# Kernel optimization log

Measured on AMD Instinct MI355X. Metric: run time of the kernel, lower is better.

Reference implementation:

```python
import jax, jax.numpy as jnp
import numpy as np


def setup_inputs() -> dict:
    key = jax.random.key(0)
    ks = jax.random.split(key, 5)
    B, c_in, c_out, style_d = 8, 128, 128, 512
    D = H = W = 32
    f = 3
    # xavier_uniform-like scale for conv weight
    fan_in = c_in * f * f * f
    fan_out = c_out * f * f * f
    limit = float(np.sqrt(6.0 / (fan_in + fan_out)))
    x = jax.random.normal(ks[0], (B, c_in, D, H, W), dtype=jnp.float32)
    s = jax.random.normal(ks[1], (B, style_d), dtype=jnp.float32)
    w = jax.random.uniform(ks[2], (c_out, c_in, f, f, f), dtype=jnp.float32, minval=-limit, maxval=limit)
    b = jnp.zeros((c_out, 1, 1, 1), dtype=jnp.float32)
    lim_a = float(np.sqrt(1.0 / style_d))
    affine_w = jax.random.uniform(ks[3], (c_in, style_d), dtype=jnp.float32, minval=-lim_a, maxval=lim_a)
    affine_b = jnp.zeros((c_in,), dtype=jnp.float32)
    return {"x": x, "s": s, "w": w, "b": b, "affine_w": affine_w, "affine_b": affine_b}


def _per_sample_conv(xi, wi):
    # xi: [c_in, D, H, W], wi: [c_out, c_in, 3, 3, 3]
    out = jax.lax.conv_general_dilated(
        xi[None],  # [1, c_in, D, H, W]
        wi,
        window_strides=(1, 1, 1),
        padding=((1, 1), (1, 1), (1, 1)),
        dimension_numbers=("NCDHW", "OIDHW", "NCDHW"),
    )
    return out[0]  # [c_out, D, H, W]


def reference(x, s, w, b, affine_w, affine_b):
    # Style -> per-sample channel scales
    style = s @ affine_w.T + affine_b  # [B, c_in]
    # Modulate: [B, c_out, c_in, f, f, f]
    wmod = w[None] * (style[:, None, :, None, None, None] + 1.0)
    # Demodulate
    d = jnp.sqrt(jnp.sum(jnp.square(wmod), axis=(2, 3, 4, 5), keepdims=True) + 1e-8)
    wmod = wmod / d
    # Per-sample conv (equivalent to grouped conv with groups=B)
    out = jax.vmap(_per_sample_conv)(x, wmod)  # [B, c_out, D, H, W]
    return out + b[None]
```

## Files before the change

kernel.cpp:

```cpp
#include <hip/hip_runtime.h>
#include <stdint.h>
#include <stddef.h>

typedef __attribute__((ext_vector_type(8))) short short8;
typedef __attribute__((ext_vector_type(4))) float floatx4;

#define CI 128
#define CO 128
#define SP 32768
#define BATCH 8
#define STYLED 512
#define KV 3456

__device__ __forceinline__ short f2bf(float f) {
    uint32_t u = __builtin_bit_cast(uint32_t, f);
    u = (u + 0x7FFFu + ((u >> 16) & 1u)) >> 16;
    return (short)(u & 0xFFFFu);
}

__global__ void k_style(const float* __restrict__ s, const float* __restrict__ aw,
                        const float* __restrict__ ab, float* __restrict__ m) {
    __shared__ float ssh[STYLED];
    int b = blockIdx.x;
    int i = threadIdx.x;
    for (int r = 0; r < STYLED / 128; ++r) ssh[r * 128 + i] = s[b * STYLED + r * 128 + i];
    __syncthreads();
    float acc = ab[i] + 1.0f;
    const float4* awr = (const float4*)(aw + (size_t)i * STYLED);
    for (int d4 = 0; d4 < STYLED / 4; ++d4) {
        float4 v = awr[d4];
        acc += v.x * ssh[d4 * 4] + v.y * ssh[d4 * 4 + 1] + v.z * ssh[d4 * 4 + 2] + v.w * ssh[d4 * 4 + 3];
    }
    m[b * CI + i] = acc;
}

__global__ void k_wmod(const float* __restrict__ w, const float* __restrict__ m,
                       short* __restrict__ wt) {
    int b = blockIdx.x >> 7;
    int o = blockIdx.x & 127;
    int lane = threadIdx.x;
    const float* wrow = w + (size_t)o * KV;
    const float* mrow = m + b * CI;
    float sum = 0.f;
    for (int e = lane; e < KV; e += 64) {
        int i = e / 27;
        float v = wrow[e] * mrow[i];
        sum += v * v;
    }
    #pragma unroll
    for (int off = 32; off >= 1; off >>= 1) sum += __shfl_xor(sum, off);
    float scale = 1.0f / sqrtf(sum + 1e-8f);
    for (int e = lane; e < KV; e += 64) {
        int i = e / 27;
        int k = e - i * 27;
        float v = wrow[e] * mrow[i] * scale;
        wt[(((size_t)(b * 27 + k) * CO + o) << 7) + i] = f2bf(v);
    }
}

__global__ void k_xt(const float* __restrict__ x, short* __restrict__ xt) {
    __shared__ float t[128][33];
    int bid = blockIdx.x;
    int b = bid >> 10;
    int zy = bid & 1023;
    const float* src = x + (size_t)b * CI * SP + (size_t)zy * 32;
    int tid = threadIdx.x;
    int wlane = tid & 31, irow = tid >> 5;
    for (int it = 0; it < 16; ++it) {
        int i = it * 8 + irow;
        t[i][wlane] = src[(size_t)i * SP + wlane];
    }
    __syncthreads();
    short* dst = xt + ((size_t)(b * SP + zy * 32)) * CI;
    for (int it = 0; it < 2; ++it) {
        int idx = it * 256 + tid;
        int wv = idx >> 4, g = idx & 15;
        short8 v;
        #pragma unroll
        for (int j = 0; j < 8; ++j) v[j] = f2bf(t[g * 8 + j][wv]);
        *(short8*)(dst + (size_t)wv * CI + g * 8) = v;
    }
}

__launch_bounds__(512, 1)
__global__ void k_conv(const short* __restrict__ xt, const short* __restrict__ wt,
                       const float* __restrict__ bias, float* __restrict__ out) {
    __shared__ short lds_x[612 * 40];
    __shared__ short lds_w[2][128 * 40];

    int bid = blockIdx.x;
    int b = bid & 7;
    int t = bid >> 3;
    int z = t & 31;
    int y0 = (t >> 5) * 4;
    int tid = threadIdx.x;
    int lane = tid & 63;
    int wid = tid >> 6;
    int wm = wid & 3;
    int wn = wid >> 2;
    int l15 = lane & 15;
    int lhi = lane >> 4;
    int i8 = lhi * 8;

    floatx4 acc[2][4];
    #pragma unroll
    for (int a = 0; a < 2; ++a)
        #pragma unroll
        for (int c = 0; c < 4; ++c) acc[a][c] = (floatx4){0.f, 0.f, 0.f, 0.f};

    const short* wbase = wt + (size_t)b * 27 * CO * CI;
    int wo = tid >> 2, wq = tid & 3;

    for (int c = 0; c < 4; ++c) {
        __syncthreads();
        for (int it = 0; it < 5; ++it) {
            int idx = it * 512 + tid;
            if (idx < 2448) {
                int h = idx >> 2, q = idx & 3;
                int zh = h / 204; int r = h - zh * 204;
                int yh = r / 34;  int wh = r - yh * 34;
                int zz = z + zh - 1, yy = y0 + yh - 1, ww = wh - 1;
                short8 v = {0, 0, 0, 0, 0, 0, 0, 0};
                if ((unsigned)zz < 32u && (unsigned)yy < 32u && (unsigned)ww < 32u) {
                    v = *(const short8*)(xt + ((size_t)(b * SP + zz * 1024 + yy * 32 + ww)) * CI + c * 32 + q * 8);
                }
                *(short8*)&lds_x[h * 40 + q * 8] = v;
            }
        }
        {
            short8 v = *(const short8*)(wbase + ((size_t)0 * CO + wo) * CI + c * 32 + wq * 8);
            *(short8*)&lds_w[0][wo * 40 + wq * 8] = v;
        }
        __syncthreads();

        for (int tap = 0; tap < 27; ++tap) {
            short8 wreg;
            if (tap < 26) {
                wreg = *(const short8*)(wbase + ((size_t)(tap + 1) * CO + wo) * CI + c * 32 + wq * 8);
            }
            int cur = tap & 1;
            int kd = tap / 9, r9 = tap - kd * 9;
            int kh = r9 / 3, kw = r9 - kh * 3;

            short8 afr[2];
            #pragma unroll
            for (int mf = 0; mf < 2; ++mf)
                afr[mf] = *(const short8*)&lds_w[cur][(wm * 32 + mf * 16 + l15) * 40 + i8];

            #pragma unroll
            for (int nf = 0; nf < 4; ++nf) {
                int n = wn * 64 + nf * 16;
                int yi = n >> 5;
                int wl = (n & 31) + l15;
                int h = (kd * 6 + yi + kh) * 34 + wl + kw;
                short8 bfr = *(const short8*)&lds_x[h * 40 + i8];
                #pragma unroll
                for (int mf = 0; mf < 2; ++mf)
                    acc[mf][nf] = __builtin_amdgcn_mfma_f32_16x16x32_bf16(afr[mf], bfr, acc[mf][nf], 0, 0, 0);
            }

            if (tap < 26) {
                __syncthreads();
                *(short8*)&lds_w[cur ^ 1][wo * 40 + wq * 8] = wreg;
                __syncthreads();
            }
        }
    }

    float bv[2][4];
    #pragma unroll
    for (int mf = 0; mf < 2; ++mf)
        #pragma unroll
        for (int j = 0; j < 4; ++j)
            bv[mf][j] = bias[wm * 32 + mf * 16 + lhi * 4 + j];

    #pragma unroll
    for (int mf = 0; mf < 2; ++mf) {
        int o = wm * 32 + mf * 16 + lhi * 4;
        #pragma unroll
        for (int nf = 0; nf < 4; ++nf) {
            int n = wn * 64 + nf * 16 + l15;
            int yy = y0 + (n >> 5);
            int ww = n & 31;
            size_t obase = ((size_t)(b * CO + o)) * SP + (size_t)z * 1024 + yy * 32 + ww;
            #pragma unroll
            for (int j = 0; j < 4; ++j)
                out[obase + (size_t)j * SP] = acc[mf][nf][j] + bv[mf][j];
        }
    }
}

extern "C" void kernel_launch(void* const* d_in, const int* in_sizes, int n_in,
                              void* d_out, int out_size, void* d_ws, size_t ws_size,
                              hipStream_t stream) {
    const float* x  = (const float*)d_in[0];
    const float* s  = (const float*)d_in[1];
    const float* w  = (const float*)d_in[2];
    const float* bb = (const float*)d_in[3];
    const float* aw = (const float*)d_in[4];
    const float* ab = (const float*)d_in[5];
    float* out = (float*)d_out;

    float* style_m = (float*)d_ws;
    short* wmodT   = (short*)((char*)d_ws + 4096);
    short* xT      = (short*)((char*)d_ws + 4096 + 7077888);

    k_style<<<BATCH, 128, 0, stream>>>(s, aw, ab, style_m);
    k_wmod<<<BATCH * CO, 64, 0, stream>>>(w, style_m, wmodT);
    k_xt<<<BATCH * 1024, 256, 0, stream>>>(x, xT);
    k_conv<<<BATCH * 256, 512, 0, stream>>>(xT, wmodT, bb, out);
}
```

Measured before the change: 359.0 us.

## Use direct global-to-LDS loads with XOR swizzle and larger conv tiles

The conv kernel now fills LDS with global_load_lds DMA-style loads instead of going through registers. Padding reads are redirected to a zeroed page, and XOR-swizzled layouts for both weights and activations replace the padded-stride scheme to avoid bank conflicts. The weight buffer is re-laid out per 32-channel chunk to match. Each block now covers two z-slices, each warp computes 64x64 instead of 32x64, and the two barriers per tap become one. This raises register pressure and leaves half as many blocks, in exchange for more data reuse and fewer VGPR round trips.

Result: faster. 295.9 us (-17.6%).

```diff
diff --git a/kernel.cpp b/kernel.cpp
--- a/kernel.cpp
+++ b/kernel.cpp
@@ -11,6 +11,13 @@
 #define BATCH 8
 #define STYLED 512
 #define KV 3456
+
+typedef __attribute__((address_space(1))) const void gvoid_t;
+typedef __attribute__((address_space(3))) void lvoid_t;
+
+__device__ __forceinline__ void gload16(const void* g, void* l) {
+    __builtin_amdgcn_global_load_lds((gvoid_t*)g, (lvoid_t*)l, 16, 0, 0);
+}
 
 __device__ __forceinline__ short f2bf(float f) {
     uint32_t u = __builtin_bit_cast(uint32_t, f);
@@ -50,11 +57,14 @@
     #pragma unroll
     for (int off = 32; off >= 1; off >>= 1) sum += __shfl_xor(sum, off);
     float scale = 1.0f / sqrtf(sum + 1e-8f);
+    int ophase = (o >> 1) & 3;
     for (int e = lane; e < KV; e += 64) {
         int i = e / 27;
         int k = e - i * 27;
         float v = wrow[e] * mrow[i] * scale;
-        wt[(((size_t)(b * 27 + k) * CO + o) << 7) + i] = f2bf(v);
+        int c = i >> 5, il = i & 31, g = il >> 3, r = il & 7;
+        int gl = g ^ ophase;
+        wt[(((size_t)((b * 4 + c) * 27 + k)) * 128 + o) * 32 + gl * 8 + r] = f2bf(v);
     }
 }
 
@@ -82,107 +92,102 @@
     }
 }
 
-__launch_bounds__(512, 1)
+__launch_bounds__(512, 4)
 __global__ void k_conv(const short* __restrict__ xt, const short* __restrict__ wt,
-                       const float* __restrict__ bias, float* __restrict__ out) {
-    __shared__ short lds_x[612 * 40];
-    __shared__ short lds_w[2][128 * 40];
+                       const float* __restrict__ bias, float* __restrict__ out,
+                       const short* __restrict__ zeropage) {
+    __shared__ short lds_x[816 * 32];
+    __shared__ short lds_w[2][128 * 32];
 
     int bid = blockIdx.x;
     int b = bid & 7;
     int t = bid >> 3;
-    int z = t & 31;
-    int y0 = (t >> 5) * 4;
+    int zt = t & 15, yt = t >> 4;
+    int z0 = zt * 2, y0 = yt * 4;
+
     int tid = threadIdx.x;
     int lane = tid & 63;
     int wid = tid >> 6;
-    int wm = wid & 3;
-    int wn = wid >> 2;
+    int wm = wid >> 2;
+    int wn = wid & 3;
     int l15 = lane & 15;
     int lhi = lane >> 4;
-    int i8 = lhi * 8;
-
-    floatx4 acc[2][4];
-    #pragma unroll
-    for (int a = 0; a < 2; ++a)
+
+    floatx4 acc[4][4];
+    #pragma unroll
+    for (int a = 0; a < 4; ++a)
         #pragma unroll
         for (int c = 0; c < 4; ++c) acc[a][c] = (floatx4){0.f, 0.f, 0.f, 0.f};
 
-    const short* wbase = wt + (size_t)b * 27 * CO * CI;
-    int wo = tid >> 2, wq = tid & 3;
+    const short* wb = wt + (size_t)b * (4 * 27 * 128 * 32);
+    const short* xb = xt + (size_t)b * SP * CI;
 
     for (int c = 0; c < 4; ++c) {
+        for (int j = 0; ; ++j) {
+            int s = wid + 8 * j;
+            if (s >= 51) break;
+            int G = s * 64 + lane;
+            int rowid = G >> 2, g = G & 3;
+            int zh = rowid / 204; int rr = rowid - zh * 204;
+            int yh = rr / 34;     int wh = rr - yh * 34;
+            int zz = z0 + zh - 1, yy = y0 + yh - 1, ww = wh - 1;
+            int q = g ^ ((rowid >> 1) & 3);
+            const short* src;
+            if ((unsigned)zz < 32u && (unsigned)yy < 32u && (unsigned)ww < 32u)
+                src = xb + ((size_t)(zz * 1024 + yy * 32 + ww)) * CI + c * 32 + q * 8;
+            else
+                src = zeropage + q * 8;
+            gload16(src, (void*)((char*)lds_x + s * 1024));
+        }
+        gload16(wb + ((size_t)(c * 27 + 0)) * 4096 + wid * 512 + lane * 8,
+                (void*)((char*)lds_w[0] + wid * 1024));
         __syncthreads();
-        for (int it = 0; it < 5; ++it) {
-            int idx = it * 512 + tid;
-            if (idx < 2448) {
-                int h = idx >> 2, q = idx & 3;
-                int zh = h / 204; int r = h - zh * 204;
-                int yh = r / 34;  int wh = r - yh * 34;
-                int zz = z + zh - 1, yy = y0 + yh - 1, ww = wh - 1;
-                short8 v = {0, 0, 0, 0, 0, 0, 0, 0};
-                if ((unsigned)zz < 32u && (unsigned)yy < 32u && (unsigned)ww < 32u) {
-                    v = *(const short8*)(xt + ((size_t)(b * SP + zz * 1024 + yy * 32 + ww)) * CI + c * 32 + q * 8);
-                }
-                *(short8*)&lds_x[h * 40 + q * 8] = v;
-            }
-        }
-        {
-            short8 v = *(const short8*)(wbase + ((size_t)0 * CO + wo) * CI + c * 32 + wq * 8);
-            *(short8*)&lds_w[0][wo * 40 + wq * 8] = v;
-        }
-        __syncthreads();
 
         for (int tap = 0; tap < 27; ++tap) {
-            short8 wreg;
-            if (tap < 26) {
-                wreg = *(const short8*)(wbase + ((size_t)(tap + 1) * CO + wo) * CI + c * 32 + wq * 8);
-            }
             int cur = tap & 1;
+            if (tap < 26)
+                gload16(wb + ((size_t)(c * 27 + tap + 1)) * 4096 + wid * 512 + lane * 8,
+                        (void*)((char*)lds_w[cur ^ 1] + wid * 1024));
             int kd = tap / 9, r9 = tap - kd * 9;
             int kh = r9 / 3, kw = r9 - kh * 3;
 
-            short8 afr[2];
+            short8 af[4];
             #pragma unroll
-            for (int mf = 0; mf < 2; ++mf)
-                afr[mf] = *(const short8*)&lds_w[cur][(wm * 32 + mf * 16 + l15) * 40 + i8];
-
+            for (int mf = 0; mf < 4; ++mf) {
+                int o = wm * 64 + mf * 16 + l15;
+                af[mf] = *(const short8*)((const char*)lds_w[cur] + o * 64 +
+                                          ((lhi ^ ((o >> 1) & 3)) << 4));
+            }
             #pragma unroll
             for (int nf = 0; nf < 4; ++nf) {
                 int n = wn * 64 + nf * 16;
-                int yi = n >> 5;
-                int wl = (n & 31) + l15;
-                int h = (kd * 6 + yi + kh) * 34 + wl + kw;
-                short8 bfr = *(const short8*)&lds_x[h * 40 + i8];
+                int zi = n >> 7, yi = (n >> 5) & 3;
+                int h = ((zi + kd) * 6 + (yi + kh)) * 34 + (n & 31) + kw + l15;
+                short8 bf = *(const short8*)((const char*)lds_x + h * 64 +
+                                             ((lhi ^ ((h >> 1) & 3)) << 4));
                 #pragma unroll
-                for (int mf = 0; mf < 2; ++mf)
-                    acc[mf][nf] = __builtin_amdgcn_mfma_f32_16x16x32_bf16(afr[mf], bfr, acc[mf][nf], 0, 0, 0);
+                for (int mf = 0; mf < 4; ++mf)
+                    acc[mf][nf] = __builtin_amdgcn_mfma_f32_16x16x32_bf16(af[mf], bf, acc[mf][nf], 0, 0, 0);
             }
-
-            if (tap < 26) {
-                __syncthreads();
-                *(short8*)&lds_w[cur ^ 1][wo * 40 + wq * 8] = wreg;
-                __syncthreads();
-            }
+            __syncthreads();
         }
     }
 
-    float bv[2][4];
-    #pragma unroll
-    for (int mf = 0; mf < 2; ++mf)
+    float bv[4][4];
+    #pragma unroll
+    for (int mf = 0; mf < 4; ++mf)
         #pragma unroll
         for (int j = 0; j < 4; ++j)
-            bv[mf][j] = bias[wm * 32 + mf * 16 + lhi * 4 + j];
-
-    #pragma unroll
-    for (int mf = 0; mf < 2; ++mf) {
-        int o = wm * 32 + mf * 16 + lhi * 4;
+            bv[mf][j] = bias[wm * 64 + mf * 16 + lhi * 4 + j];
+
+    #pragma unroll
+    for (int mf = 0; mf < 4; ++mf) {
+        int o = wm * 64 + mf * 16 + lhi * 4;
         #pragma unroll
         for (int nf = 0; nf < 4; ++nf) {
-            int n = wn * 64 + nf * 16 + l15;
-            int yy = y0 + (n >> 5);
-            int ww = n & 31;
-            size_t obase = ((size_t)(b * CO + o)) * SP + (size_t)z * 1024 + yy * 32 + ww;
+            int n = wn * 64 + nf * 16;
+            int zi = n >> 7, yi = (n >> 5) & 3, wcol = (n & 31) + l15;
+            size_t obase = ((size_t)(b * CO + o)) * SP + (size_t)(z0 + zi) * 1024 + (y0 + yi) * 32 + wcol;
             #pragma unroll
             for (int j = 0; j < 4; ++j)
                 out[obase + (size_t)j * SP] = acc[mf][nf][j] + bv[mf][j];
@@ -204,9 +209,11 @@
     float* style_m = (float*)d_ws;
     short* wmodT   = (short*)((char*)d_ws + 4096);
     short* xT      = (short*)((char*)d_ws + 4096 + 7077888);
-
+    short* zpage   = (short*)((char*)d_ws + 4096 + 7077888 + 67108864);
+
+    hipMemsetAsync(zpage, 0, 256, stream);
     k_style<<<BATCH, 128, 0, stream>>>(s, aw, ab, style_m);
     k_wmod<<<BATCH * CO, 64, 0, stream>>>(w, style_m, wmodT);
     k_xt<<<BATCH * 1024, 256, 0, stream>>>(x, xT);
-    k_conv<<<BATCH * 256, 512, 0, stream>>>(xT, wmodT, bb, out);
-}
+    k_conv<<<BATCH * 128, 512, 0, stream>>>(xT, wmodT, bb, out, zpage);
+}
```

## Restructure conv into 4x4x32 tiles with full-tap weight chunks and 32x32 MFMA

Applied to the files above, without the earlier changes.

The conv kernel now computes a 4x4x32 output tile per block, so there are 64 blocks per sample instead of 256. Each 16-channel chunk loads all 27 taps of weights into LDS at once, with register prefetch and global_load_lds direct copies, replacing the per-tap double-buffer that needed two barriers per tap. It also switches to 32x32x16 bf16 MFMA with larger accumulators, and the weight layout and x transpose kernel change to match. The aim is fewer barriers and more halo reuse, at the cost of more registers, larger LDS use and fewer blocks in the grid.

After: 629.2 us. 75.3% more time.

```diff
diff --git a/kernel.cpp b/kernel.cpp
--- a/kernel.cpp
+++ b/kernel.cpp
@@ -3,7 +3,7 @@
 #include <stddef.h>
 
 typedef __attribute__((ext_vector_type(8))) short short8;
-typedef __attribute__((ext_vector_type(4))) float floatx4;
+typedef __attribute__((ext_vector_type(16))) float f32x16;
 
 #define CI 128
 #define CO 128
@@ -12,6 +12,16 @@
 #define STYLED 512
 #define KV 3456
 
+#define WGR 6912
+#define XGR 2448
+#define WCHUNK_BYTES (WGR * 16)
+
+typedef __attribute__((address_space(1))) const void gvoid_t;
+typedef __attribute__((address_space(3))) void lvoid_t;
+__device__ __forceinline__ void gload16(const void* g, void* l) {
+    __builtin_amdgcn_global_load_lds((gvoid_t*)g, (lvoid_t*)l, 16, 0, 0);
+}
+
 __device__ __forceinline__ short f2bf(float f) {
     uint32_t u = __builtin_bit_cast(uint32_t, f);
     u = (u + 0x7FFFu + ((u >> 16) & 1u)) >> 16;
@@ -19,10 +29,12 @@
 }
 
 __global__ void k_style(const float* __restrict__ s, const float* __restrict__ aw,
-                        const float* __restrict__ ab, float* __restrict__ m) {
+                        const float* __restrict__ ab, float* __restrict__ m,
+                        float* __restrict__ zp) {
     __shared__ float ssh[STYLED];
     int b = blockIdx.x;
     int i = threadIdx.x;
+    if (b == 0 && i < 64) zp[i] = 0.f;
     for (int r = 0; r < STYLED / 128; ++r) ssh[r * 128 + i] = s[b * STYLED + r * 128 + i];
     __syncthreads();
     float acc = ab[i] + 1.0f;
@@ -54,140 +66,162 @@
         int i = e / 27;
         int k = e - i * 27;
         float v = wrow[e] * mrow[i] * scale;
-        wt[(((size_t)(b * 27 + k) * CO + o) << 7) + i] = f2bf(v);
+        int c = i >> 4, cl = i & 15;
+        wt[(((size_t)(b * 8 + c) * 27 + k) * 128 + o) * 16 + cl] = f2bf(v);
     }
 }
 
 __global__ void k_xt(const float* __restrict__ x, short* __restrict__ xt) {
-    __shared__ float t[128][33];
     int bid = blockIdx.x;
-    int b = bid >> 10;
-    int zy = bid & 1023;
-    const float* src = x + (size_t)b * CI * SP + (size_t)zy * 32;
-    int tid = threadIdx.x;
-    int wlane = tid & 31, irow = tid >> 5;
-    for (int it = 0; it < 16; ++it) {
-        int i = it * 8 + irow;
-        t[i][wlane] = src[(size_t)i * SP + wlane];
-    }
-    __syncthreads();
-    short* dst = xt + ((size_t)(b * SP + zy * 32)) * CI;
-    for (int it = 0; it < 2; ++it) {
-        int idx = it * 256 + tid;
-        int wv = idx >> 4, g = idx & 15;
-        short8 v;
-        #pragma unroll
-        for (int j = 0; j < 8; ++j) v[j] = f2bf(t[g * 8 + j][wv]);
-        *(short8*)(dst + (size_t)wv * CI + g * 8) = v;
-    }
-}
-
-__launch_bounds__(512, 1)
+    int b = bid >> 9, c = (bid >> 7) & 3, spb = bid & 127;
+    int sp = spb * 256 + threadIdx.x;
+    const float* src = x + ((size_t)(b * CI + c * 32)) * SP + sp;
+    float f[32];
+    #pragma unroll
+    for (int ch = 0; ch < 32; ++ch) f[ch] = src[(size_t)ch * SP];
+    short8 v[4];
+    #pragma unroll
+    for (int q = 0; q < 4; ++q)
+        #pragma unroll
+        for (int j = 0; j < 8; ++j) v[q][j] = f2bf(f[q * 8 + j]);
+    short* dst = xt + (size_t)(b * SP + sp) * CI + c * 32;
+    #pragma unroll
+    for (int q = 0; q < 4; ++q) *(short8*)(dst + q * 8) = v[q];
+}
+
+__launch_bounds__(512, 2)
 __global__ void k_conv(const short* __restrict__ xt, const short* __restrict__ wt,
-                       const float* __restrict__ bias, float* __restrict__ out) {
-    __shared__ short lds_x[612 * 40];
-    __shared__ short lds_w[2][128 * 40];
+                       const float* __restrict__ bias, float* __restrict__ out,
+                       const short* __restrict__ zp) {
+    __shared__ short lds[(WGR + XGR) * 8];
 
     int bid = blockIdx.x;
     int b = bid & 7;
-    int t = bid >> 3;
-    int z = t & 31;
-    int y0 = (t >> 5) * 4;
-    int tid = threadIdx.x;
-    int lane = tid & 63;
-    int wid = tid >> 6;
-    int wm = wid & 3;
-    int wn = wid >> 2;
-    int l15 = lane & 15;
-    int lhi = lane >> 4;
-    int i8 = lhi * 8;
-
-    floatx4 acc[2][4];
-    #pragma unroll
-    for (int a = 0; a < 2; ++a)
-        #pragma unroll
-        for (int c = 0; c < 4; ++c) acc[a][c] = (floatx4){0.f, 0.f, 0.f, 0.f};
-
-    const short* wbase = wt + (size_t)b * 27 * CO * CI;
-    int wo = tid >> 2, wq = tid & 3;
-
-    for (int c = 0; c < 4; ++c) {
+    int s = bid >> 3;
+    int z0 = (s & 7) * 4, y0 = (s >> 3) * 4;
+    int tid = threadIdx.x, lane = tid & 63, wid = tid >> 6;
+    int wm = wid >> 2;
+    int wn = wid & 3;
+    int l31 = lane & 31, g = lane >> 5;
+
+    const char* xb = (const char*)(xt + (size_t)b * SP * CI);
+    const char* wb = (const char*)wt + (size_t)b * 8 * WCHUNK_BYTES;
+
+    int xoff[5];
+    #pragma unroll
+    for (int j = 0; j < 5; ++j) {
+        int gx = tid + 512 * j;
+        int row = gx >> 1, half = gx & 1;
+        int zh = row / 204, r2 = row - zh * 204;
+        int yh = r2 / 34, wh = r2 - yh * 34;
+        int zz = z0 + zh - 1, yy = y0 + yh - 1, ww = wh - 1;
+        bool ok = (gx < XGR) && ((unsigned)zz < 32u) && ((unsigned)yy < 32u) && ((unsigned)ww < 32u);
+        xoff[j] = ok ? ((zz * 1024 + yy * 32 + ww) * CI * 2 + half * 16) : -1;
+    }
+
+    f32x16 acc[2][4];
+    #pragma unroll
+    for (int mf = 0; mf < 2; ++mf)
+        #pragma unroll
+        for (int nf = 0; nf < 4; ++nf)
+            #pragma unroll
+            for (int e = 0; e < 16; ++e) acc[mf][nf][e] = 0.f;
+
+    short8 wreg[7], xreg[5];
+    #pragma unroll
+    for (int k = 0; k < 7; ++k)
+        wreg[k] = *(const short8*)(wb + (tid + 512 * k) * 16);
+    #pragma unroll
+    for (int j = 0; j < 5; ++j)
+        if (tid + 512 * j < XGR) {
+            const char* src = (xoff[j] >= 0) ? (xb + xoff[j]) : (const char*)zp;
+            xreg[j] = *(const short8*)src;
+        }
+
+    #pragma unroll 1
+    for (int c = 0; c < 8; ++c) {
         __syncthreads();
-        for (int it = 0; it < 5; ++it) {
-            int idx = it * 512 + tid;
-            if (idx < 2448) {
-                int h = idx >> 2, q = idx & 3;
-                int zh = h / 204; int r = h - zh * 204;
-                int yh = r / 34;  int wh = r - yh * 34;
-                int zz = z + zh - 1, yy = y0 + yh - 1, ww = wh - 1;
-                short8 v = {0, 0, 0, 0, 0, 0, 0, 0};
-                if ((unsigned)zz < 32u && (unsigned)yy < 32u && (unsigned)ww < 32u) {
-                    v = *(const short8*)(xt + ((size_t)(b * SP + zz * 1024 + yy * 32 + ww)) * CI + c * 32 + q * 8);
+        #pragma unroll
+        for (int k = 0; k < 7; ++k)
+            *(short8*)&lds[(tid + 512 * k) * 8] = wreg[k];
+        #pragma unroll
+        for (int j = 0; j < 5; ++j)
+            if (tid + 512 * j < XGR)
+                *(short8*)&lds[(WGR + tid + 512 * j) * 8] = xreg[j];
+        __syncthreads();
+
+        const char* wbc = wb + (size_t)c * WCHUNK_BYTES;
+        #pragma unroll
+        for (int j2 = 0; j2 < 7; ++j2) {
+            int i = wid + 8 * j2;
+            if (i < 52)
+                gload16(wbc + (3584 + i * 64 + lane) * 16,
+                        (void*)((char*)lds + (3584 + i * 64) * 16));
+        }
+        if (c < 7) {
+            const char* wbn = wbc + WCHUNK_BYTES;
+            #pragma unroll
+            for (int k = 0; k < 7; ++k)
+                wreg[k] = *(const short8*)(wbn + (tid + 512 * k) * 16);
+            #pragma unroll
+            for (int j = 0; j < 5; ++j)
+                if (tid + 512 * j < XGR) {
+                    const char* src = (xoff[j] >= 0) ? (xb + xoff[j] + (c + 1) * 32)
+                                                     : (const char*)zp;
+                    xreg[j] = *(const short8*)src;
                 }
-                *(short8*)&lds_x[h * 40 + q * 8] = v;
-            }
-        }
-        {
-            short8 v = *(const short8*)(wbase + ((size_t)0 * CO + wo) * CI + c * 32 + wq * 8);
-            *(short8*)&lds_w[0][wo * 40 + wq * 8] = v;
-        }
-        __syncthreads();
-
-        for (int tap = 0; tap < 27; ++tap) {
-            short8 wreg;
-            if (tap < 26) {
-                wreg = *(const short8*)(wbase + ((size_t)(tap + 1) * CO + wo) * CI + c * 32 + wq * 8);
-            }
-            int cur = tap & 1;
+        }
+
+        #pragma unroll
+        for (int tap = 0; tap < 14; ++tap) {
             int kd = tap / 9, r9 = tap - kd * 9;
             int kh = r9 / 3, kw = r9 - kh * 3;
-
-            short8 afr[2];
+            short8 af[2];
             #pragma unroll
             for (int mf = 0; mf < 2; ++mf)
-                afr[mf] = *(const short8*)&lds_w[cur][(wm * 32 + mf * 16 + l15) * 40 + i8];
-
+                af[mf] = *(const short8*)&lds[(tap * 128 + wm * 64 + mf * 32 + l31) * 16 + g * 8];
             #pragma unroll
             for (int nf = 0; nf < 4; ++nf) {
-                int n = wn * 64 + nf * 16;
-                int yi = n >> 5;
-                int wl = (n & 31) + l15;
-                int h = (kd * 6 + yi + kh) * 34 + wl + kw;
-                short8 bfr = *(const short8*)&lds_x[h * 40 + i8];
-                #pragma unroll
-                for (int mf = 0; mf < 2; ++mf)
-                    acc[mf][nf] = __builtin_amdgcn_mfma_f32_16x16x32_bf16(afr[mf], bfr, acc[mf][nf], 0, 0, 0);
+                int row = (wn + kd) * 204 + (nf + kh) * 34 + l31 + kw;
+                short8 bf = *(const short8*)&lds[WGR * 8 + row * 16 + g * 8];
+                acc[0][nf] = __builtin_amdgcn_mfma_f32_32x32x16_bf16(af[0], bf, acc[0][nf], 0, 0, 0);
+                acc[1][nf] = __builtin_amdgcn_mfma_f32_32x32x16_bf16(af[1], bf, acc[1][nf], 0, 0, 0);
             }
-
-            if (tap < 26) {
-                __syncthreads();
-                *(short8*)&lds_w[cur ^ 1][wo * 40 + wq * 8] = wreg;
-                __syncthreads();
+        }
+
+        __syncthreads();
+
+        #pragma unroll
+        for (int tap = 14; tap < 27; ++tap) {
+            int kd = tap / 9, r9 = tap - kd * 9;
+            int kh = r9 / 3, kw = r9 - kh * 3;
+            short8 af[2];
+            #pragma unroll
+            for (int mf = 0; mf < 2; ++mf)
+                af[mf] = *(const short8*)&lds[(tap * 128 + wm * 64 + mf * 32 + l31) * 16 + g * 8];
+            #pragma unroll
+            for (int nf = 0; nf < 4; ++nf) {
+                int row = (wn + kd) * 204 + (nf + kh) * 34 + l31 + kw;
+                short8 bf = *(const short8*)&lds[WGR * 8 + row * 16 + g * 8];
+                acc[0][nf] = __builtin_amdgcn_mfma_f32_32x32x16_bf16(af[0], bf, acc[0][nf], 0, 0, 0);
+                acc[1][nf] = __builtin_amdgcn_mfma_f32_32x32x16_bf16(af[1], bf, acc[1][nf], 0, 0, 0);
             }
         }
     }
 
-    float bv[2][4];
+    size_t ob = (size_t)b * CO * SP;
     #pragma unroll
     for (int mf = 0; mf < 2; ++mf)
         #pragma unroll
-        for (int j = 0; j < 4; ++j)
-            bv[mf][j] = bias[wm * 32 + mf * 16 + lhi * 4 + j];
-
-    #pragma unroll
-    for (int mf = 0; mf < 2; ++mf) {
-        int o = wm * 32 + mf * 16 + lhi * 4;
-        #pragma unroll
         for (int nf = 0; nf < 4; ++nf) {
-            int n = wn * 64 + nf * 16 + l15;
-            int yy = y0 + (n >> 5);
-            int ww = n & 31;
-            size_t obase = ((size_t)(b * CO + o)) * SP + (size_t)z * 1024 + yy * 32 + ww;
-            #pragma unroll
-            for (int j = 0; j < 4; ++j)
-                out[obase + (size_t)j * SP] = acc[mf][nf][j] + bv[mf][j];
-        }
-    }
+            int z = z0 + wn, y = y0 + nf;
+            size_t base = ob + (size_t)z * 1024 + y * 32 + l31;
+            #pragma unroll
+            for (int j = 0; j < 16; ++j) {
+                int co = wm * 64 + mf * 32 + (j & 3) + 8 * (j >> 2) + 4 * g;
+                out[base + (size_t)co * SP] = acc[mf][nf][j] + bias[co];
+            }
+        }
 }
 
 extern "C" void kernel_launch(void* const* d_in, const int* in_sizes, int n_in,
@@ -204,9 +238,10 @@
     float* style_m = (float*)d_ws;
     short* wmodT   = (short*)((char*)d_ws + 4096);
     short* xT      = (short*)((char*)d_ws + 4096 + 7077888);
-
-    k_style<<<BATCH, 128, 0, stream>>>(s, aw, ab, style_m);
+    float* zpage   = (float*)((char*)d_ws + 4096 + 7077888 + 67108864);
+
+    k_style<<<BATCH, 128, 0, stream>>>(s, aw, ab, style_m, zpage);
     k_wmod<<<BATCH * CO, 64, 0, stream>>>(w, style_m, wmodT);
-    k_xt<<<BATCH * 1024, 256, 0, stream>>>(x, xT);
-    k_conv<<<BATCH * 256, 512, 0, stream>>>(xT, wmodT, bb, out);
-}
+    k_xt<<<BATCH * 4 * 128, 256, 0, stream>>>(x, xT);
+    k_conv<<<BATCH * 64, 512, 0, stream>>>(xT, wmodT, bb, out, (const short*)zpage);
+}
```
